# Kernel tuning notes

Hardware: AMD Instinct MI355X
Metric: run time of the kernel (lower is better)

The kernel has to match this reference:

```python
import jax, jax.numpy as jnp
import numpy as np


def setup_inputs() -> dict:
    key = jax.random.key(0)
    k_x, k_rbf, k_nb, k_w1, k_w2 = jax.random.split(key, 5)
    N, NB, F_DIM, RBF_DIM = 20000, 32, 128, 64
    x = jax.random.normal(k_x, (N, F_DIM), dtype=jnp.float32)
    rbf = jax.random.uniform(k_rbf, (N, NB, RBF_DIM), dtype=jnp.float32)
    neighbors = jax.random.randint(k_nb, (N, NB), 0, N, dtype=jnp.int64)
    # filter network params (Linear(rbf_dim->f_dim), Softplus, Linear(f_dim->f_dim))
    w1 = jax.random.normal(k_w1, (RBF_DIM, F_DIM), dtype=jnp.float32) / np.sqrt(RBF_DIM)
    b1 = jnp.zeros((F_DIM,), dtype=jnp.float32)
    w2 = jax.random.normal(k_w2, (F_DIM, F_DIM), dtype=jnp.float32) / np.sqrt(F_DIM)
    b2 = jnp.zeros((F_DIM,), dtype=jnp.float32)
    return {"x": x, "rbf": rbf, "neighbors": neighbors,
            "w1": w1, "b1": b1, "w2": w2, "b2": b2}


def reference(x, rbf, neighbors, w1, b1, w2, b2):
    # filter network: Linear -> Softplus -> Linear, applied per (atom, neighbor)
    h = jax.nn.softplus(jnp.einsum('anr,rf->anf', rbf, w1) + b1)  # [N, NB, F]
    W = jnp.einsum('ang,gf->anf', h, w2) + b2                      # [N, NB, F]
    x_j = x[neighbors]                                             # gather [N, NB, F]
    return jnp.sum(x_j * W, axis=1)                                # [N, F]
```

## Files before the change

kernel.cpp:

```cpp
#include <hip/hip_runtime.h>
#include <hip/hip_bf16.h>
#include <math.h>


#define NB     32
#define FD     128
#define RD     64
#define WAVES  8
#define NTILES 2500

#define LOG2E 1.4426950408889634f
#define LN2   0.6931471805599453f

typedef short  short8  __attribute__((ext_vector_type(8)));
typedef float  floatx4 __attribute__((ext_vector_type(4)));
typedef float  floatx2 __attribute__((ext_vector_type(2)));

#define LDS_FENCE() asm volatile("" ::: "memory")

static __device__ __forceinline__ unsigned pk2(float a, float b) {
  __hip_bfloat162 h = __float22bfloat162_rn(float2{a, b});
  unsigned u;
  __builtin_memcpy(&u, &h, sizeof(u));
  return u;
}

static __device__ __forceinline__ float sp2(float acc) {
  return __builtin_amdgcn_logf(1.0f + __builtin_amdgcn_exp2f(acc));
}

__global__ __launch_bounds__(512, 4)
void cfconv_kernel(const float* __restrict__ x,
                   const float* __restrict__ rbf,
                   const int*   __restrict__ nbr,
                   const float* __restrict__ w1,
                   const float* __restrict__ b1,
                   const float* __restrict__ w2,
                   const float* __restrict__ b2,
                   float* __restrict__ out) {
  __shared__ __align__(16) short w1f[16][64][8];
  __shared__ __align__(16) short w2f[32][64][8];
  __shared__ __align__(16) short hbuf[WAVES * 16][128];

  const int tid  = threadIdx.x;
  const int lane = tid & 63;
  const int wv   = tid >> 6;
  const int q    = lane >> 4;
  const int ln   = lane & 15;

  for (int i = tid; i < RD * FD; i += 512) {
    int k = i >> 7, n = i & 127, kk = k & 31;
    w1f[(k >> 5) * 8 + (n >> 4)][(kk >> 3) * 16 + (n & 15)][kk & 7] =
        (short)pk2(w1[i] * LOG2E, 0.f);
  }
  for (int i = tid; i < FD * FD; i += 512) {
    int k = i >> 7, n = i & 127, kk = k & 31;
    w2f[(k >> 5) * 8 + (n >> 4)][(kk >> 3) * 16 + (n & 15)][kk & 7] =
        (short)pk2(w2[i] * LN2, 0.f);
  }
  float b1v[8], b2v[8];
#pragma unroll
  for (int nt = 0; nt < 8; ++nt) {
    b1v[nt] = b1[nt * 16 + ln] * LOG2E;
    b2v[nt] = b2[nt * 16 + ln];
  }
  __syncthreads();

  short (*band)[128] = &hbuf[wv * 16];
  const int cb2 = (lane * 2) >> 3;
  const int cl2 = (lane * 2) & 7;

  for (int tile = blockIdx.x; tile < NTILES; tile += gridDim.x) {
    const int atom = tile * WAVES + wv;
    const int prow = atom * NB;
    const int* nbp = nbr + prow;

    float o0 = 0.f, o1 = 0.f;

#pragma unroll
    for (int mt = 0; mt < 2; ++mt) {
      const float* src = rbf + (prow + mt * 16 + ln) * RD + q * 8;
      short8 afrag[2];
#pragma unroll
      for (int kt = 0; kt < 2; ++kt) {
        floatx4 lo = __builtin_nontemporal_load((const floatx4*)(src + kt * 32));
        floatx4 hi = __builtin_nontemporal_load((const floatx4*)(src + kt * 32 + 4));
        union { short8 s8; unsigned u[4]; } f;
        f.u[0] = pk2(lo[0], lo[1]);
        f.u[1] = pk2(lo[2], lo[3]);
        f.u[2] = pk2(hi[0], hi[1]);
        f.u[3] = pk2(hi[2], hi[3]);
        afrag[kt] = f.s8;
      }

      floatx4 acc[8];
#pragma unroll
      for (int nt = 0; nt < 8; ++nt) acc[nt] = floatx4{0.f, 0.f, 0.f, 0.f};
#pragma unroll
      for (int kt = 0; kt < 2; ++kt)
#pragma unroll
        for (int nt = 0; nt < 8; ++nt) {
          short8 bfrag = *(const short8*)&w1f[kt * 8 + nt][lane][0];
          acc[nt] = __builtin_amdgcn_mfma_f32_16x16x32_bf16(
              afrag[kt], bfrag, acc[nt], 0, 0, 0);
        }

#pragma unroll
      for (int nt = 0; nt < 8; ++nt) {
        const int c  = nt * 16 + ln;
        const int cb = c >> 3, cl = c & 7;
        unsigned u01 = pk2(sp2(acc[nt][0] + b1v[nt]), sp2(acc[nt][1] + b1v[nt]));
        unsigned u23 = pk2(sp2(acc[nt][2] + b1v[nt]), sp2(acc[nt][3] + b1v[nt]));
        band[q * 4 + 0][(((cb ^ (q * 4 + 0)) & 15) << 3) | cl] = (short)u01;
        band[q * 4 + 1][(((cb ^ (q * 4 + 1)) & 15) << 3) | cl] = (short)(u01 >> 16);
        band[q * 4 + 2][(((cb ^ (q * 4 + 2)) & 15) << 3) | cl] = (short)u23;
        band[q * 4 + 3][(((cb ^ (q * 4 + 3)) & 15) << 3) | cl] = (short)(u23 >> 16);
      }
      LDS_FENCE();

      short8 hfrag[4];
#pragma unroll
      for (int kt = 0; kt < 4; ++kt) {
        const int pb = ((kt * 4 + q) ^ ln) & 15;
        hfrag[kt] = *(const short8*)&band[ln][pb << 3];
      }
      LDS_FENCE();

#pragma unroll
      for (int nt = 0; nt < 8; ++nt) acc[nt] = floatx4{0.f, 0.f, 0.f, 0.f};
#pragma unroll
      for (int kt = 0; kt < 4; ++kt)
#pragma unroll
        for (int nt = 0; nt < 8; ++nt) {
          short8 bfrag = *(const short8*)&w2f[kt * 8 + nt][lane][0];
          acc[nt] = __builtin_amdgcn_mfma_f32_16x16x32_bf16(
              hfrag[kt], bfrag, acc[nt], 0, 0, 0);
        }

#pragma unroll
      for (int nt = 0; nt < 8; ++nt) {
        const int c  = nt * 16 + ln;
        const int cb = c >> 3, cl = c & 7;
        unsigned u01 = pk2(acc[nt][0] + b2v[nt], acc[nt][1] + b2v[nt]);
        unsigned u23 = pk2(acc[nt][2] + b2v[nt], acc[nt][3] + b2v[nt]);
        band[q * 4 + 0][(((cb ^ (q * 4 + 0)) & 15) << 3) | cl] = (short)u01;
        band[q * 4 + 1][(((cb ^ (q * 4 + 1)) & 15) << 3) | cl] = (short)(u01 >> 16);
        band[q * 4 + 2][(((cb ^ (q * 4 + 2)) & 15) << 3) | cl] = (short)u23;
        band[q * 4 + 3][(((cb ^ (q * 4 + 3)) & 15) << 3) | cl] = (short)(u23 >> 16);
      }
      LDS_FENCE();

#pragma unroll 4
      for (int r = 0; r < 16; ++r) {
        const int j = nbp[mt * 16 + r];
        floatx2 xv = *(const floatx2*)(x + j * FD + lane * 2);
        unsigned pw;
        __builtin_memcpy(&pw, &band[r][(((cb2 ^ r) & 15) << 3) | cl2], 4);
        o0 = fmaf(xv[0], __builtin_bit_cast(float, pw << 16), o0);
        o1 = fmaf(xv[1], __builtin_bit_cast(float, pw & 0xFFFF0000u), o1);
      }
      LDS_FENCE();
    }

    __builtin_nontemporal_store(floatx2{o0, o1}, (floatx2*)(out + atom * FD + lane * 2));
  }
}

extern "C" void kernel_launch(void* const* d_in, const int* in_sizes, int n_in,
                              void* d_out, int out_size, void* d_ws, size_t ws_size,
                              hipStream_t stream) {
  const float* x   = (const float*)d_in[0];
  const float* rbf = (const float*)d_in[1];
  const int*   nbr = (const int*)d_in[2];
  const float* w1  = (const float*)d_in[3];
  const float* b1  = (const float*)d_in[4];
  const float* w2  = (const float*)d_in[5];
  const float* b2  = (const float*)d_in[6];
  float* out = (float*)d_out;

  cfconv_kernel<<<dim3(500), dim3(512), 0, stream>>>(x, rbf, nbr, w1, b1, w2, b2, out);
}
```

Measured before the change: 288.2 us.

## Transpose first MFMA and consume second MFMA output directly in registers

The first GEMM now has its operands swapped so the softplus output lands in a layout that packs into 64-bit LDS writes, and the bias is folded into the accumulator's initial value. The second GEMM's output is no longer staged through LDS. Each lane multiplies its accumulator entries directly with gathered x rows, using neighbor indices loaded as an int4, and the four quads are reduced with cross-lane shuffles at the end. This removes one LDS round trip and its bf16 rounding of the filter weights, but gather loads become scalar 4-byte accesses strided by 16 floats and register pressure rises.

```diff
diff --git a/kernel.cpp b/kernel.cpp
--- a/kernel.cpp
+++ b/kernel.cpp
@@ -15,6 +15,7 @@
 typedef short  short8  __attribute__((ext_vector_type(8)));
 typedef float  floatx4 __attribute__((ext_vector_type(4)));
 typedef float  floatx2 __attribute__((ext_vector_type(2)));
+typedef int    intx4   __attribute__((ext_vector_type(4)));
 
 #define LDS_FENCE() asm volatile("" ::: "memory")
 
@@ -40,7 +41,7 @@
                    float* __restrict__ out) {
   __shared__ __align__(16) short w1f[16][64][8];
   __shared__ __align__(16) short w2f[32][64][8];
-  __shared__ __align__(16) short hbuf[WAVES * 16][128];
+  __shared__ __align__(16) unsigned long long hb[WAVES][16][32];
 
   const int tid  = threadIdx.x;
   const int lane = tid & 63;
@@ -58,29 +59,29 @@
     w2f[(k >> 5) * 8 + (n >> 4)][(kk >> 3) * 16 + (n & 15)][kk & 7] =
         (short)pk2(w2[i] * LN2, 0.f);
   }
-  float b1v[8], b2v[8];
+  float b2v[8];
 #pragma unroll
-  for (int nt = 0; nt < 8; ++nt) {
-    b1v[nt] = b1[nt * 16 + ln] * LOG2E;
-    b2v[nt] = b2[nt * 16 + ln];
-  }
+  for (int nt = 0; nt < 8; ++nt) b2v[nt] = b2[nt * 16 + ln];
   __syncthreads();
 
-  short (*band)[128] = &hbuf[wv * 16];
-  const int cb2 = (lane * 2) >> 3;
-  const int cl2 = (lane * 2) & 7;
+  unsigned long long (*band)[32] = hb[wv];
+  const int swz = ln ^ ((ln & 2) << 3);
 
   for (int tile = blockIdx.x; tile < NTILES; tile += gridDim.x) {
     const int atom = tile * WAVES + wv;
     const int prow = atom * NB;
     const int* nbp = nbr + prow;
 
-    float o0 = 0.f, o1 = 0.f;
+    float o[8];
+#pragma unroll
+    for (int nt = 0; nt < 8; ++nt) o[nt] = 0.f;
 
 #pragma unroll
     for (int mt = 0; mt < 2; ++mt) {
-      const float* src = rbf + (prow + mt * 16 + ln) * RD + q * 8;
-      short8 afrag[2];
+      const intx4 nbi = *(const intx4*)(nbp + mt * 16 + q * 4);
+
+      const float* src = rbf + (size_t)(prow + mt * 16 + ln) * RD + q * 8;
+      short8 bfr[2];
 #pragma unroll
       for (int kt = 0; kt < 2; ++kt) {
         floatx4 lo = __builtin_nontemporal_load((const floatx4*)(src + kt * 32));
@@ -90,79 +91,92 @@
         f.u[1] = pk2(lo[2], lo[3]);
         f.u[2] = pk2(hi[0], hi[1]);
         f.u[3] = pk2(hi[2], hi[3]);
-        afrag[kt] = f.s8;
+        bfr[kt] = f.s8;
       }
 
       floatx4 acc[8];
 #pragma unroll
-      for (int nt = 0; nt < 8; ++nt) acc[nt] = floatx4{0.f, 0.f, 0.f, 0.f};
+      for (int nt = 0; nt < 8; ++nt) {
+        floatx4 bv = *(const floatx4*)(b1 + nt * 16 + q * 4);
+        acc[nt] = floatx4{bv[0] * LOG2E, bv[1] * LOG2E, bv[2] * LOG2E, bv[3] * LOG2E};
+      }
 #pragma unroll
       for (int kt = 0; kt < 2; ++kt)
 #pragma unroll
         for (int nt = 0; nt < 8; ++nt) {
-          short8 bfrag = *(const short8*)&w1f[kt * 8 + nt][lane][0];
-          acc[nt] = __builtin_amdgcn_mfma_f32_16x16x32_bf16(
-              afrag[kt], bfrag, acc[nt], 0, 0, 0);
+          short8 afr = *(const short8*)&w1f[kt * 8 + nt][lane][0];
+          acc[nt] = __builtin_amdgcn_mfma_f32_16x16x32_bf16(afr, bfr[kt], acc[nt], 0, 0, 0);
         }
 
 #pragma unroll
       for (int nt = 0; nt < 8; ++nt) {
-        const int c  = nt * 16 + ln;
-        const int cb = c >> 3, cl = c & 7;
-        unsigned u01 = pk2(sp2(acc[nt][0] + b1v[nt]), sp2(acc[nt][1] + b1v[nt]));
-        unsigned u23 = pk2(sp2(acc[nt][2] + b1v[nt]), sp2(acc[nt][3] + b1v[nt]));
-        band[q * 4 + 0][(((cb ^ (q * 4 + 0)) & 15) << 3) | cl] = (short)u01;
-        band[q * 4 + 1][(((cb ^ (q * 4 + 1)) & 15) << 3) | cl] = (short)(u01 >> 16);
-        band[q * 4 + 2][(((cb ^ (q * 4 + 2)) & 15) << 3) | cl] = (short)u23;
-        band[q * 4 + 3][(((cb ^ (q * 4 + 3)) & 15) << 3) | cl] = (short)(u23 >> 16);
+        unsigned u0 = pk2(sp2(acc[nt][0]), sp2(acc[nt][1]));
+        unsigned u1 = pk2(sp2(acc[nt][2]), sp2(acc[nt][3]));
+        unsigned long long v = (unsigned long long)u0 | ((unsigned long long)u1 << 32);
+        band[ln][(nt * 4 + q) ^ swz] = v;
       }
       LDS_FENCE();
 
-      short8 hfrag[4];
+      short8 hfr[4];
 #pragma unroll
       for (int kt = 0; kt < 4; ++kt) {
-        const int pb = ((kt * 4 + q) ^ ln) & 15;
-        hfrag[kt] = *(const short8*)&band[ln][pb << 3];
+        union { short8 s8; unsigned long long d[2]; } f;
+        f.d[0] = band[ln][(kt * 8 + q * 2)     ^ swz];
+        f.d[1] = band[ln][(kt * 8 + q * 2 + 1) ^ swz];
+        hfr[kt] = f.s8;
       }
       LDS_FENCE();
 
+      const float* xb0 = x + (size_t)nbi[0] * FD + ln;
+      float xa[8], xc[8];
 #pragma unroll
-      for (int nt = 0; nt < 8; ++nt) acc[nt] = floatx4{0.f, 0.f, 0.f, 0.f};
+      for (int nt = 0; nt < 8; ++nt) xa[nt] = xb0[nt * 16];
+
+#pragma unroll
+      for (int nt = 0; nt < 8; ++nt)
+        acc[nt] = floatx4{b2v[nt], b2v[nt], b2v[nt], b2v[nt]};
 #pragma unroll
       for (int kt = 0; kt < 4; ++kt)
 #pragma unroll
         for (int nt = 0; nt < 8; ++nt) {
-          short8 bfrag = *(const short8*)&w2f[kt * 8 + nt][lane][0];
-          acc[nt] = __builtin_amdgcn_mfma_f32_16x16x32_bf16(
-              hfrag[kt], bfrag, acc[nt], 0, 0, 0);
+          short8 bfr2 = *(const short8*)&w2f[kt * 8 + nt][lane][0];
+          acc[nt] = __builtin_amdgcn_mfma_f32_16x16x32_bf16(hfr[kt], bfr2, acc[nt], 0, 0, 0);
         }
 
+      const float* xb1 = x + (size_t)nbi[1] * FD + ln;
 #pragma unroll
-      for (int nt = 0; nt < 8; ++nt) {
-        const int c  = nt * 16 + ln;
-        const int cb = c >> 3, cl = c & 7;
-        unsigned u01 = pk2(acc[nt][0] + b2v[nt], acc[nt][1] + b2v[nt]);
-        unsigned u23 = pk2(acc[nt][2] + b2v[nt], acc[nt][3] + b2v[nt]);
-        band[q * 4 + 0][(((cb ^ (q * 4 + 0)) & 15) << 3) | cl] = (short)u01;
-        band[q * 4 + 1][(((cb ^ (q * 4 + 1)) & 15) << 3) | cl] = (short)(u01 >> 16);
-        band[q * 4 + 2][(((cb ^ (q * 4 + 2)) & 15) << 3) | cl] = (short)u23;
-        band[q * 4 + 3][(((cb ^ (q * 4 + 3)) & 15) << 3) | cl] = (short)(u23 >> 16);
-      }
-      LDS_FENCE();
+      for (int nt = 0; nt < 8; ++nt) xc[nt] = xb1[nt * 16];
+#pragma unroll
+      for (int nt = 0; nt < 8; ++nt) o[nt] = fmaf(xa[nt], acc[nt][0], o[nt]);
 
-#pragma unroll 4
-      for (int r = 0; r < 16; ++r) {
-        const int j = nbp[mt * 16 + r];
-        floatx2 xv = *(const floatx2*)(x + j * FD + lane * 2);
-        unsigned pw;
-        __builtin_memcpy(&pw, &band[r][(((cb2 ^ r) & 15) << 3) | cl2], 4);
-        o0 = fmaf(xv[0], __builtin_bit_cast(float, pw << 16), o0);
-        o1 = fmaf(xv[1], __builtin_bit_cast(float, pw & 0xFFFF0000u), o1);
-      }
-      LDS_FENCE();
+      const float* xb2 = x + (size_t)nbi[2] * FD + ln;
+#pragma unroll
+      for (int nt = 0; nt < 8; ++nt) xa[nt] = xb2[nt * 16];
+#pragma unroll
+      for (int nt = 0; nt < 8; ++nt) o[nt] = fmaf(xc[nt], acc[nt][1], o[nt]);
+
+      const float* xb3 = x + (size_t)nbi[3] * FD + ln;
+#pragma unroll
+      for (int nt = 0; nt < 8; ++nt) xc[nt] = xb3[nt * 16];
+#pragma unroll
+      for (int nt = 0; nt < 8; ++nt) o[nt] = fmaf(xa[nt], acc[nt][2], o[nt]);
+
+#pragma unroll
+      for (int nt = 0; nt < 8; ++nt) o[nt] = fmaf(xc[nt], acc[nt][3], o[nt]);
     }
 
-    __builtin_nontemporal_store(floatx2{o0, o1}, (floatx2*)(out + atom * FD + lane * 2));
+#pragma unroll
+    for (int nt = 0; nt < 8; ++nt) {
+      o[nt] += __shfl_xor(o[nt], 16);
+      o[nt] += __shfl_xor(o[nt], 32);
+    }
+    float s0 = o[0], s1 = o[1];
+    if (q == 1) { s0 = o[2]; s1 = o[3]; }
+    if (q == 2) { s0 = o[4]; s1 = o[5]; }
+    if (q == 3) { s0 = o[6]; s1 = o[7]; }
+    float* op = out + (size_t)atom * FD + q * 32 + ln;
+    __builtin_nontemporal_store(s0, op);
+    __builtin_nontemporal_store(s1, op + 16);
   }
 }
 
```

Measured after the change: 418.4 us. 1.45x slower.
